# Optimization experiments

Measured on AMD Instinct MI355X. Metric: run time of the kernel, lower is better.

The kernel has to match this reference:

```python
import jax, jax.numpy as jnp
import numpy as np

NEG_NUM = -10000.0


def setup_inputs() -> dict:
    key = jax.random.key(0)
    k1, k2, k3 = jax.random.split(key, 3)
    B, S, T, D = 8, 4096, 512, 1024
    ctx = jax.random.normal(k1, (B, S, D), dtype=jnp.float32)
    query = jax.random.normal(k2, (B, T, D), dtype=jnp.float32)
    mask = jax.random.randint(k3, (B, S), 0, 2, dtype=jnp.int32)
    return {"ctx": ctx, "query": query, "mask": mask}


def reference(ctx, query, mask):
    # ctx: [B, S, D], query: [B, T, D], mask: [B, S] (0 = masked)
    D = query.shape[-1]
    denom = jnp.asarray(np.sqrt(D), dtype=ctx.dtype)
    # scores[b, t, s] = sum_d query[b, t, d] * ctx[b, s, d]
    scores = jnp.einsum("btd,bsd->bts", query, ctx) / denom
    # apply mask per source position (broadcast over target dim)
    scores = jnp.where(mask[:, None, :] == 0, NEG_NUM, scores)
    p_ctx = jax.nn.softmax(scores, axis=-1)  # [B, T, S]
    expected_ctx = jnp.einsum("bts,bsd->btd", p_ctx, ctx)  # [B, T, D]
    return expected_ctx, p_ctx
```

## Files before the change

kernel.cpp:

```cpp
#include <hip/hip_runtime.h>

#define BB 8
#define SS 4096
#define TT 512
#define DD 1024

typedef __attribute__((ext_vector_type(8))) short bf16x8;
typedef __attribute__((ext_vector_type(4))) short bf16x4;
typedef __attribute__((ext_vector_type(4))) float f32x4;

#define GLOAD_LDS16(gp, lp)                                            \
  __builtin_amdgcn_global_load_lds(                                    \
      (const __attribute__((address_space(1))) void*)(gp),             \
      (__attribute__((address_space(3))) void*)(lp), 16, 0, 0)

__device__ inline unsigned short f2bf(float f) {
  unsigned int u = __float_as_uint(f);
  u += 0x7FFFu + ((u >> 16) & 1u);
  return (unsigned short)(u >> 16);
}
__device__ inline void pack16(const float* __restrict__ src, short* __restrict__ dst) {
  f32x4 f0 = *(const f32x4*)(src + 0);
  f32x4 f1 = *(const f32x4*)(src + 4);
  f32x4 f2 = *(const f32x4*)(src + 8);
  f32x4 f3 = *(const f32x4*)(src + 12);
  bf16x8 b0, b1;
  b0[0] = (short)f2bf(f0.x); b0[1] = (short)f2bf(f0.y);
  b0[2] = (short)f2bf(f0.z); b0[3] = (short)f2bf(f0.w);
  b0[4] = (short)f2bf(f1.x); b0[5] = (short)f2bf(f1.y);
  b0[6] = (short)f2bf(f1.z); b0[7] = (short)f2bf(f1.w);
  b1[0] = (short)f2bf(f2.x); b1[1] = (short)f2bf(f2.y);
  b1[2] = (short)f2bf(f2.z); b1[3] = (short)f2bf(f2.w);
  b1[4] = (short)f2bf(f3.x); b1[5] = (short)f2bf(f3.y);
  b1[6] = (short)f2bf(f3.z); b1[7] = (short)f2bf(f3.w);
  *(bf16x8*)(dst + 0) = b0;
  *(bf16x8*)(dst + 8) = b1;
}

#define WS_NEED ((size_t)168 << 20)
#define OFF_QB  ((size_t)0)
#define OFF_CB  ((size_t)8 << 20)
#define OFF_CT  ((size_t)72 << 20)
#define OFF_PB  ((size_t)136 << 20)
#define OFF_PART ((size_t)0)

__global__ __launch_bounds__(256) void prep_q_kernel(const float* __restrict__ q,
                                                     short* __restrict__ qb) {
  const size_t idx = ((size_t)blockIdx.x * 256 + threadIdx.x) * 16;
  pack16(q + idx, qb + idx);
}

__global__ __launch_bounds__(256) void prep_c_kernel(const float* __restrict__ c,
                                                     short* __restrict__ cb,
                                                     short* __restrict__ ct) {
  const int b  = blockIdx.z;
  const int s0 = blockIdx.y * 128;
  const int d0 = blockIdx.x * 64;
  const float* C = c + (size_t)b * SS * DD;
  __shared__ float T[128 * 64];

  const int tid = threadIdx.x;
  const int r0 = tid >> 4;
  const int cc = tid & 15;

  f32x4 v[8];
#pragma unroll
  for (int i = 0; i < 8; ++i)
    v[i] = *(const f32x4*)(C + (size_t)(s0 + r0 + i * 16) * DD + d0 + cc * 4);

#pragma unroll
  for (int i = 0; i < 8; ++i) {
    const int r = r0 + i * 16;
    bf16x4 o;
    o[0] = (short)f2bf(v[i].x); o[1] = (short)f2bf(v[i].y);
    o[2] = (short)f2bf(v[i].z); o[3] = (short)f2bf(v[i].w);
    *(bf16x4*)(cb + (size_t)b * SS * DD + (size_t)(s0 + r) * DD + d0 + cc * 4) = o;
    *(f32x4*)&T[r * 64 + ((cc ^ (r >> 3)) & 15) * 4] = v[i];
  }
  __syncthreads();

  const int sc  = (tid & 15) * 8;
  const int dr0 = tid >> 4;
#pragma unroll
  for (int i = 0; i < 4; ++i) {
    const int d = dr0 + i * 16;
    bf16x8 o;
#pragma unroll
    for (int j = 0; j < 8; ++j) {
      const int s = sc + j;
      o[j] = (short)f2bf(T[s * 64 + (((d >> 2) ^ (s >> 3)) & 15) * 4 + (d & 3)]);
    }
    *(bf16x8*)(ct + (size_t)b * DD * SS + (size_t)(d0 + d) * SS + s0 + sc) = o;
  }
}


__global__ __launch_bounds__(256) void qk_kernel_f(const short* __restrict__ qb,
                                                   const short* __restrict__ cb,
                                                   const int* __restrict__ mask,
                                                   float* __restrict__ p) {
  const int b  = blockIdx.z;
  const int m0 = blockIdx.y * 128;
  const int n0 = blockIdx.x * 128;
  const short* A  = qb + (size_t)b * TT * DD;
  const short* Bt = cb + (size_t)b * SS * DD;

  __shared__ alignas(16) short As[2][128 * 64];
  __shared__ alignas(16) short Bs[2][128 * 64];

  const int tid  = threadIdx.x;
  const int wave = tid >> 6, lane = tid & 63;
  const int quad = lane >> 4, l16 = lane & 15;
  const int wm = (wave >> 1) * 64, wn = (wave & 1) * 64;

  const int rl = lane >> 3;
  const int ck = (lane & 7) ^ (lane >> 3);
  const int x7 = l16 & 7;

  f32x4 acc[4][4];
#pragma unroll
  for (int i = 0; i < 4; ++i)
#pragma unroll
    for (int j = 0; j < 4; ++j) acc[i][j] = (f32x4){0.f, 0.f, 0.f, 0.f};

#define QK_STAGE(buf, k0)                                                     \
  {                                                                           \
    _Pragma("unroll")                                                         \
    for (int t = 0; t < 4; ++t) {                                             \
      const int rb = wave * 32 + t * 8;                                       \
      GLOAD_LDS16(A  + (size_t)(m0 + rb + rl) * DD + (k0) + ck * 8,           \
                  &As[buf][rb * 64]);                                         \
      GLOAD_LDS16(Bt + (size_t)(n0 + rb + rl) * DD + (k0) + ck * 8,           \
                  &Bs[buf][rb * 64]);                                         \
    }                                                                         \
  }

#define QK_COMPUTE(buf)                                                       \
  {                                                                           \
    _Pragma("unroll")                                                         \
    for (int kk = 0; kk < 2; ++kk) {                                          \
      bf16x8 af[4], bfv[4];                                                   \
      _Pragma("unroll")                                                       \
      for (int i = 0; i < 4; ++i)                                             \
        af[i] = *(const bf16x8*)&As[buf][(wm + i * 16 + l16) * 64 +           \
                                        (((kk * 4 + quad) ^ x7) * 8)];        \
      _Pragma("unroll")                                                       \
      for (int j = 0; j < 4; ++j)                                             \
        bfv[j] = *(const bf16x8*)&Bs[buf][(wn + j * 16 + l16) * 64 +          \
                                          (((kk * 4 + quad) ^ x7) * 8)];      \
      _Pragma("unroll")                                                       \
      for (int i = 0; i < 4; ++i)                                             \
        _Pragma("unroll")                                                     \
        for (int j = 0; j < 4; ++j)                                           \
          acc[i][j] = __builtin_amdgcn_mfma_f32_16x16x32_bf16(                \
              af[i], bfv[j], acc[i][j], 0, 0, 0);                             \
    }                                                                         \
  }

  QK_STAGE(0, 0);
  __syncthreads();
  int cur = 0;
  for (int k0 = 64; k0 < DD; k0 += 64) {
    QK_STAGE(cur ^ 1, k0);
    QK_COMPUTE(cur);
    __syncthreads();
    cur ^= 1;
  }
  QK_COMPUTE(cur);

  float* P = p + (size_t)b * TT * SS;
  int mk[4];
#pragma unroll
  for (int j = 0; j < 4; ++j) mk[j] = mask[b * SS + n0 + wn + j * 16 + l16];
#pragma unroll
  for (int i = 0; i < 4; ++i)
#pragma unroll
    for (int j = 0; j < 4; ++j)
#pragma unroll
      for (int r = 0; r < 4; ++r) {
        const int row = m0 + wm + i * 16 + quad * 4 + r;
        const int col = n0 + wn + j * 16 + l16;
        const float val = (mk[j] == 0) ? -10000.0f : acc[i][j][r] * 0.03125f;
        P[(size_t)row * SS + col] = val;
      }
}

__global__ __launch_bounds__(256) void softmax_kernel_f(float* __restrict__ p,
                                                        short* __restrict__ pb) {
  const int wave = threadIdx.x >> 6, lane = threadIdx.x & 63;
  const int row = blockIdx.x * 4 + wave;
  float* pr = p + (size_t)row * SS;
  short* pbr = pb + (size_t)row * SS;

  f32x4 v[16];
  float mx = -3.0e38f;
#pragma unroll
  for (int h = 0; h < 16; ++h) {
    v[h] = *(const f32x4*)(pr + h * 256 + lane * 4);
    mx = fmaxf(mx, fmaxf(fmaxf(v[h].x, v[h].y), fmaxf(v[h].z, v[h].w)));
  }
#pragma unroll
  for (int off = 32; off > 0; off >>= 1) mx = fmaxf(mx, __shfl_xor(mx, off));

  float sum = 0.f;
#pragma unroll
  for (int h = 0; h < 16; ++h) {
    v[h].x = __expf(v[h].x - mx);
    v[h].y = __expf(v[h].y - mx);
    v[h].z = __expf(v[h].z - mx);
    v[h].w = __expf(v[h].w - mx);
    sum += (v[h].x + v[h].y) + (v[h].z + v[h].w);
  }
#pragma unroll
  for (int off = 32; off > 0; off >>= 1) sum += __shfl_xor(sum, off);
  const float inv = 1.0f / sum;

#pragma unroll
  for (int h = 0; h < 16; ++h) {
    f32x4 o;
    o.x = v[h].x * inv; o.y = v[h].y * inv;
    o.z = v[h].z * inv; o.w = v[h].w * inv;
    *(f32x4*)(pr + h * 256 + lane * 4) = o;
    bf16x4 ob;
    ob[0] = (short)f2bf(o.x); ob[1] = (short)f2bf(o.y);
    ob[2] = (short)f2bf(o.z); ob[3] = (short)f2bf(o.w);
    *(bf16x4*)(pbr + h * 256 + lane * 4) = ob;
  }
}

__global__ __launch_bounds__(256) void pv_kernel_f(const short* __restrict__ pb,
                                                   const short* __restrict__ ct,
                                                   float* __restrict__ part) {
  const int n0 = blockIdx.x * 128;
  const int m0 = blockIdx.y * 128;
  const int z  = blockIdx.z;
  const int b  = z >> 1;
  const int ks = z & 1;
  const short* A  = pb + (size_t)b * TT * SS;
  const short* Bt = ct + (size_t)b * DD * SS;

  __shared__ alignas(16) short As[2][128 * 64];
  __shared__ alignas(16) short Bs[2][128 * 64];

  const int tid  = threadIdx.x;
  const int wave = tid >> 6, lane = tid & 63;
  const int quad = lane >> 4, l16 = lane & 15;
  const int wm = (wave >> 1) * 64, wn = (wave & 1) * 64;

  const int rl = lane >> 3;
  const int ck = (lane & 7) ^ (lane >> 3);
  const int x7 = l16 & 7;

  f32x4 acc[4][4];
#pragma unroll
  for (int i = 0; i < 4; ++i)
#pragma unroll
    for (int j = 0; j < 4; ++j) acc[i][j] = (f32x4){0.f, 0.f, 0.f, 0.f};

#define PV_STAGE(buf, k0)                                                     \
  {                                                                           \
    _Pragma("unroll")                                                         \
    for (int t = 0; t < 4; ++t) {                                             \
      const int rb = wave * 32 + t * 8;                                       \
      GLOAD_LDS16(A  + (size_t)(m0 + rb + rl) * SS + (k0) + ck * 8,           \
                  &As[buf][rb * 64]);                                         \
      GLOAD_LDS16(Bt + (size_t)(n0 + rb + rl) * SS + (k0) + ck * 8,           \
                  &Bs[buf][rb * 64]);                                         \
    }                                                                         \
  }

  const int kbeg = ks * 2048;
  const int kend = kbeg + 2048;
  PV_STAGE(0, kbeg);
  __syncthreads();
  int cur = 0;
  for (int k0 = kbeg + 64; k0 < kend; k0 += 64) {
    PV_STAGE(cur ^ 1, k0);
    QK_COMPUTE(cur);
    __syncthreads();
    cur ^= 1;
  }
  QK_COMPUTE(cur);

  float* E = part + (size_t)ks * BB * TT * DD + (size_t)b * TT * DD;
#pragma unroll
  for (int i = 0; i < 4; ++i)
#pragma unroll
    for (int j = 0; j < 4; ++j)
#pragma unroll
      for (int r = 0; r < 4; ++r) {
        const int row = m0 + wm + i * 16 + quad * 4 + r;
        const int col = n0 + wn + j * 16 + l16;
        E[(size_t)row * DD + col] = acc[i][j][r];
      }
}

__global__ __launch_bounds__(256) void reduce_kernel(const float* __restrict__ part,
                                                     float* __restrict__ e) {
  const size_t idx = ((size_t)blockIdx.x * 256 + threadIdx.x) * 4;
  const size_t N = (size_t)BB * TT * DD;
  f32x4 a0 = *(const f32x4*)(part + idx);
  f32x4 a1 = *(const f32x4*)(part + N + idx);
  f32x4 o;
  o.x = a0.x + a1.x;
  o.y = a0.y + a1.y;
  o.z = a0.z + a1.z;
  o.w = a0.w + a1.w;
  *(f32x4*)(e + idx) = o;
}

__global__ __launch_bounds__(256) void qk_kernel(const float* __restrict__ q,
                                                 const float* __restrict__ c,
                                                 float* __restrict__ p) {
  const int b  = blockIdx.z;
  const int m0 = blockIdx.y * 128;
  const int n0 = blockIdx.x * 128;
  const float* A  = q + (size_t)b * TT * DD;
  const float* Bt = c + (size_t)b * SS * DD;
  __shared__ alignas(16) short As[128 * 40];
  __shared__ alignas(16) short Bs[128 * 40];
  const int tid  = threadIdx.x;
  const int wave = tid >> 6, lane = tid & 63;
  const int quad = lane >> 4, l16 = lane & 15;
  const int wm = (wave >> 1) * 64, wn = (wave & 1) * 64;
  f32x4 acc[4][4];
#pragma unroll
  for (int i = 0; i < 4; ++i)
#pragma unroll
    for (int j = 0; j < 4; ++j) acc[i][j] = (f32x4){0.f, 0.f, 0.f, 0.f};
  const int ar = tid >> 1;
  const int ak = (tid & 1) * 16;
  for (int k0 = 0; k0 < DD; k0 += 32) {
    __syncthreads();
    pack16(A  + (size_t)(m0 + ar) * DD + k0 + ak, &As[ar * 40 + ak]);
    pack16(Bt + (size_t)(n0 + ar) * DD + k0 + ak, &Bs[ar * 40 + ak]);
    __syncthreads();
    bf16x8 af[4], bfv[4];
#pragma unroll
  for (int i = 0; i < 4; ++i)
      af[i] = *(const bf16x8*)&As[(wm + i * 16 + l16) * 40 + quad * 8];
#pragma unroll
    for (int j = 0; j < 4; ++j)
      bfv[j] = *(const bf16x8*)&Bs[(wn + j * 16 + l16) * 40 + quad * 8];
#pragma unroll
    for (int i = 0; i < 4; ++i)
#pragma unroll
      for (int j = 0; j < 4; ++j)
        acc[i][j] = __builtin_amdgcn_mfma_f32_16x16x32_bf16(af[i], bfv[j],
                                                            acc[i][j], 0, 0, 0);
  }
  float* P = p + (size_t)b * TT * SS;
#pragma unroll
  for (int i = 0; i < 4; ++i)
#pragma unroll
    for (int j = 0; j < 4; ++j)
#pragma unroll
      for (int r = 0; r < 4; ++r) {
        const int row = m0 + wm + i * 16 + quad * 4 + r;
        const int col = n0 + wn + j * 16 + l16;
        P[(size_t)row * SS + col] = acc[i][j][r] * 0.03125f;
      }
}

__global__ __launch_bounds__(256) void softmax_kernel(float* __restrict__ p,
                                                      const int* __restrict__ mask) {
  const int row = blockIdx.x;
  const int b   = row >> 9;
  float* pr = p + (size_t)row * SS;
  const int* mr = mask + b * SS;
  const int tid = threadIdx.x;
  const int wave = tid >> 6, lane = tid & 63;
  float v[16];
  float mx = -3.0e38f;
#pragma unroll
  for (int h = 0; h < 4; ++h) {
    const int base = tid * 4 + h * 1024;
    f32x4 s = *(const f32x4*)(pr + base);
    const int4 m4 = *(const int4*)(mr + base);
#pragma unroll
    for (int j = 0; j < 4; ++j) {
      float f = (j == 0 ? s.x : j == 1 ? s.y : j == 2 ? s.z : s.w);
      const int mk = (j == 0 ? m4.x : j == 1 ? m4.y : j == 2 ? m4.z : m4.w);
      f = fminf(fmaxf(f, -1.0e30f), 1.0e30f);
      f = (mk == 0) ? -10000.0f : f;
      v[h * 4 + j] = f;
      mx = fmaxf(mx, f);
    }
  }
#pragma unroll
  for (int off = 32; off > 0; off >>= 1) mx = fmaxf(mx, __shfl_down(mx, off));
  __shared__ float red[4];
  if (lane == 0) red[wave] = mx;
  __syncthreads();
  mx = fmaxf(fmaxf(red[0], red[1]), fmaxf(red[2], red[3]));
  __syncthreads();
  float e[16];
  float sum = 0.f;
#pragma unroll
  for (int k = 0; k < 16; ++k) { e[k] = __expf(v[k] - mx); sum += e[k]; }
#pragma unroll
  for (int off = 32; off > 0; off >>= 1) sum += __shfl_down(sum, off);
  if (lane == 0) red[wave] = sum;
  __syncthreads();
  const float inv = 1.0f / (red[0] + red[1] + red[2] + red[3]);
#pragma unroll
  for (int h = 0; h < 4; ++h) {
    const int base = tid * 4 + h * 1024;
    f32x4 o;
    o.x = e[h * 4 + 0] * inv; o.y = e[h * 4 + 1] * inv;
    o.z = e[h * 4 + 2] * inv; o.w = e[h * 4 + 3] * inv;
    *(f32x4*)(pr + base) = o;
  }
}

__global__ __launch_bounds__(256) void pv_kernel(const float* __restrict__ p,
                                                 const float* __restrict__ c,
                                                 float* __restrict__ e) {
  const int b  = blockIdx.z;
  const int m0 = blockIdx.y * 128;
  const int n0 = blockIdx.x * 128;
  const float* A  = p + (size_t)b * TT * SS;
  const float* Bm = c + (size_t)b * SS * DD;
  __shared__ alignas(16) short As[128 * 40];
  __shared__ alignas(16) short Bs[128 * 40];
  const int tid  = threadIdx.x;
  const int wave = tid >> 6, lane = tid & 63;
  const int quad = lane >> 4, l16 = lane & 15;
  const int wm = (wave >> 1) * 64, wn = (wave & 1) * 64;
  f32x4 acc[4][4];
#pragma unroll
  for (int i = 0; i < 4; ++i)
#pragma unroll
    for (int j = 0; j < 4; ++j) acc[i][j] = (f32x4){0.f, 0.f, 0.f, 0.f};
  const int ar = tid >> 1;
  const int ak = (tid & 1) * 16;
  const int kk = tid >> 3;
  const int c0 = (tid & 7) * 16;
  for (int k0 = 0; k0 < SS; k0 += 32) {
    __syncthreads();
    pack16(A + (size_t)(m0 + ar) * SS + k0 + ak, &As[ar * 40 + ak]);
    {
      const float* bp = Bm + (size_t)(k0 + kk) * DD + n0 + c0;
#pragma unroll
      for (int h = 0; h < 4; ++h) {
        f32x4 f = *(const f32x4*)(bp + h * 4);
        Bs[(c0 + h * 4 + 0) * 40 + kk] = (short)f2bf(f.x);
        Bs[(c0 + h * 4 + 1) * 40 + kk] = (short)f2bf(f.y);
        Bs[(c0 + h * 4 + 2) * 40 + kk] = (short)f2bf(f.z);
        Bs[(c0 + h * 4 + 3) * 40 + kk] = (short)f2bf(f.w);
      }
    }
    __syncthreads();
    bf16x8 af[4], bfv[4];
#pragma unroll
    for (int i = 0; i < 4; ++i)
      af[i] = *(const bf16x8*)&As[(wm + i * 16 + l16) * 40 + quad * 8];
#pragma unroll
    for (int j = 0; j < 4; ++j)
      bfv[j] = *(const bf16x8*)&Bs[(wn + j * 16 + l16) * 40 + quad * 8];
#pragma unroll
    for (int i = 0; i < 4; ++i)
#pragma unroll
      for (int j = 0; j < 4; ++j)
        acc[i][j] = __builtin_amdgcn_mfma_f32_16x16x32_bf16(af[i], bfv[j],
                                                            acc[i][j], 0, 0, 0);
  }
  float* E = e + (size_t)b * TT * DD;
#pragma unroll
  for (int i = 0; i < 4; ++i)
#pragma unroll
    for (int j = 0; j < 4; ++j)
#pragma unroll
      for (int r = 0; r < 4; ++r) {
        const int row = m0 + wm + i * 16 + quad * 4 + r;
        const int col = n0 + wn + j * 16 + l16;
        E[(size_t)row * DD + col] = acc[i][j][r];
      }
}

extern "C" void kernel_launch(void* const* d_in, const int* in_sizes, int n_in,
                              void* d_out, int out_size, void* d_ws, size_t ws_size,
                              hipStream_t stream) {
  const float* ctx   = (const float*)d_in[0];
  const float* query = (const float*)d_in[1];
  const int*   mask  = (const int*)d_in[2];

  float* expected = (float*)d_out;
  float* p        = (float*)d_out + (size_t)BB * TT * DD;

  if (ws_size >= WS_NEED) {
    char* ws = (char*)d_ws;
    short* qb = (short*)(ws + OFF_QB);
    short* cb = (short*)(ws + OFF_CB);
    short* ct = (short*)(ws + OFF_CT);
    short* pb = (short*)(ws + OFF_PB);
    float* part = (float*)(ws + OFF_PART);

    prep_q_kernel<<<dim3((BB * TT * DD) / (256 * 16)), 256, 0, stream>>>(query, qb);
    prep_c_kernel<<<dim3(DD / 64, SS / 128, BB), 256, 0, stream>>>(ctx, cb, ct);
    qk_kernel_f<<<dim3(SS / 128, TT / 128, BB), 256, 0, stream>>>(qb, cb, mask, p);
    softmax_kernel_f<<<dim3((BB * TT) / 4), 256, 0, stream>>>(p, pb);
    pv_kernel_f<<<dim3(DD / 128, TT / 128, BB * 2), 256, 0, stream>>>(pb, ct, part);
    reduce_kernel<<<dim3((BB * TT * DD) / (256 * 4)), 256, 0, stream>>>(part, expected);
  } else {
    qk_kernel<<<dim3(SS / 128, TT / 128, BB), 256, 0, stream>>>(query, ctx, p);
    softmax_kernel<<<dim3(BB * TT), 256, 0, stream>>>(p, mask);
    pv_kernel<<<dim3(DD / 128, TT / 128, BB), 256, 0, stream>>>(p, ctx, expected);
  }
}
```

Baseline: 399.3 us.

## Drop transposed ctx copy; read row-major V via LDS transpose loads in PV

Removes the transposed bf16 copy of ctx that the prep step built and simplifies prep to a plain fp32-to-bf16 pack. The PV GEMM now stages row-major V tiles into LDS and uses ds_read_b64_tr_b16 transposing reads to form the MFMA B operand. This cuts a 64MB transposed write and its LDS transpose work, but relies on correct tr-load addressing and adds an explicit lgkmcnt wait plus a sched barrier inside the compute loop.

```diff
diff --git a/kernel.cpp b/kernel.cpp
--- a/kernel.cpp
+++ b/kernel.cpp
@@ -40,9 +40,8 @@
 #define WS_NEED ((size_t)168 << 20)
 #define OFF_QB  ((size_t)0)
 #define OFF_CB  ((size_t)8 << 20)
-#define OFF_CT  ((size_t)72 << 20)
+#define OFF_PART ((size_t)72 << 20)
 #define OFF_PB  ((size_t)136 << 20)
-#define OFF_PART ((size_t)0)
 
 __global__ __launch_bounds__(256) void prep_q_kernel(const float* __restrict__ q,
                                                      short* __restrict__ qb) {
@@ -50,48 +49,10 @@
   pack16(q + idx, qb + idx);
 }
 
-__global__ __launch_bounds__(256) void prep_c_kernel(const float* __restrict__ c,
-                                                     short* __restrict__ cb,
-                                                     short* __restrict__ ct) {
-  const int b  = blockIdx.z;
-  const int s0 = blockIdx.y * 128;
-  const int d0 = blockIdx.x * 64;
-  const float* C = c + (size_t)b * SS * DD;
-  __shared__ float T[128 * 64];
-
-  const int tid = threadIdx.x;
-  const int r0 = tid >> 4;
-  const int cc = tid & 15;
-
-  f32x4 v[8];
-#pragma unroll
-  for (int i = 0; i < 8; ++i)
-    v[i] = *(const f32x4*)(C + (size_t)(s0 + r0 + i * 16) * DD + d0 + cc * 4);
-
-#pragma unroll
-  for (int i = 0; i < 8; ++i) {
-    const int r = r0 + i * 16;
-    bf16x4 o;
-    o[0] = (short)f2bf(v[i].x); o[1] = (short)f2bf(v[i].y);
-    o[2] = (short)f2bf(v[i].z); o[3] = (short)f2bf(v[i].w);
-    *(bf16x4*)(cb + (size_t)b * SS * DD + (size_t)(s0 + r) * DD + d0 + cc * 4) = o;
-    *(f32x4*)&T[r * 64 + ((cc ^ (r >> 3)) & 15) * 4] = v[i];
-  }
-  __syncthreads();
-
-  const int sc  = (tid & 15) * 8;
-  const int dr0 = tid >> 4;
-#pragma unroll
-  for (int i = 0; i < 4; ++i) {
-    const int d = dr0 + i * 16;
-    bf16x8 o;
-#pragma unroll
-    for (int j = 0; j < 8; ++j) {
-      const int s = sc + j;
-      o[j] = (short)f2bf(T[s * 64 + (((d >> 2) ^ (s >> 3)) & 15) * 4 + (d & 3)]);
-    }
-    *(bf16x8*)(ct + (size_t)b * DD * SS + (size_t)(d0 + d) * SS + s0 + sc) = o;
-  }
+__global__ __launch_bounds__(256) void prep_cb_kernel(const float* __restrict__ c,
+                                                      short* __restrict__ cb) {
+  const size_t idx = ((size_t)blockIdx.x * 256 + threadIdx.x) * 16;
+  pack16(c + idx, cb + idx);
 }
 
 
@@ -229,18 +190,18 @@
 }
 
 __global__ __launch_bounds__(256) void pv_kernel_f(const short* __restrict__ pb,
-                                                   const short* __restrict__ ct,
+                                                   const short* __restrict__ cb,
                                                    float* __restrict__ part) {
   const int n0 = blockIdx.x * 128;
   const int m0 = blockIdx.y * 128;
   const int z  = blockIdx.z;
   const int b  = z >> 1;
   const int ks = z & 1;
-  const short* A  = pb + (size_t)b * TT * SS;
-  const short* Bt = ct + (size_t)b * DD * SS;
+  const short* A   = pb + (size_t)b * TT * SS;
+  const short* Vrm = cb + (size_t)b * SS * DD;
 
   __shared__ alignas(16) short As[2][128 * 64];
-  __shared__ alignas(16) short Bs[2][128 * 64];
+  __shared__ alignas(16) short Bs[2][64 * 128];
 
   const int tid  = threadIdx.x;
   const int wave = tid >> 6, lane = tid & 63;
@@ -250,6 +211,12 @@
   const int rl = lane >> 3;
   const int ck = (lane & 7) ^ (lane >> 3);
   const int x7 = l16 & 7;
+
+  const int rB  = (lane & 7) >> 1;
+  const int dB  = (lane >> 3) * 16 + (lane & 1) * 8;
+
+  const unsigned ldsB0 = (unsigned)(unsigned long long)&Bs[0][0];
+  const unsigned baseBq = ldsB0 + (unsigned)(quad * 2048 + (wave & 1) * 512 + l16 * 8);
 
   f32x4 acc[4][4];
 #pragma unroll
@@ -262,10 +229,41 @@
     _Pragma("unroll")                                                         \
     for (int t = 0; t < 4; ++t) {                                             \
       const int rb = wave * 32 + t * 8;                                       \
-      GLOAD_LDS16(A  + (size_t)(m0 + rb + rl) * SS + (k0) + ck * 8,           \
+      GLOAD_LDS16(A + (size_t)(m0 + rb + rl) * SS + (k0) + ck * 8,            \
                   &As[buf][rb * 64]);                                         \
-      GLOAD_LDS16(Bt + (size_t)(n0 + rb + rl) * SS + (k0) + ck * 8,           \
-                  &Bs[buf][rb * 64]);                                         \
+      const int kg = wave * 4 + t;                        \
+      GLOAD_LDS16(Vrm + (size_t)((k0) + kg * 4 + rB) * DD + n0 + dB,          \
+                  &Bs[buf][kg * 512]);                                        \
+    }                                                                         \
+  }
+
+#define PV_COMPUTE(buf)                                                       \
+  {                                                                           \
+    const unsigned bb = baseBq + (unsigned)(buf) * 16384u;                    \
+    _Pragma("unroll")                                                         \
+    for (int kk = 0; kk < 2; ++kk) {                                          \
+      bf16x8 af[4];                                                           \
+      _Pragma("unroll")                                                       \
+      for (int i = 0; i < 4; ++i)                                             \
+        af[i] = *(const bf16x8*)&As[buf][(wm + i * 16 + l16) * 64 +           \
+                                        (((kk * 4 + quad) ^ x7) * 8)];        \
+      union { struct { int2 lo, hi; } p; bf16x8 v; } bu[4];                   \
+      _Pragma("unroll")                                                       \
+      for (int j = 0; j < 4; ++j) {                                           \
+        const unsigned aj = bb + (unsigned)(kk * 8192 + j * 128);             \
+        asm volatile("ds_read_b64_tr_b16 %0, %1"                              \
+                     : "=v"(bu[j].p.lo) : "v"(aj) : "memory");                \
+        asm volatile("ds_read_b64_tr_b16 %0, %1 offset:1024"                  \
+                     : "=v"(bu[j].p.hi) : "v"(aj) : "memory");                \
+      }                                                                       \
+      asm volatile("s_waitcnt lgkmcnt(0)" ::: "memory");                      \
+      __builtin_amdgcn_sched_barrier(0);                                      \
+      _Pragma("unroll")                                                       \
+      for (int i = 0; i < 4; ++i)                                             \
+        _Pragma("unroll")                                                     \
+        for (int j = 0; j < 4; ++j)                                           \
+          acc[i][j] = __builtin_amdgcn_mfma_f32_16x16x32_bf16(                \
+              af[i], bu[j].v, acc[i][j], 0, 0, 0);                            \
     }                                                                         \
   }
 
@@ -276,11 +274,11 @@
   int cur = 0;
   for (int k0 = kbeg + 64; k0 < kend; k0 += 64) {
     PV_STAGE(cur ^ 1, k0);
-    QK_COMPUTE(cur);
+    PV_COMPUTE(cur);
     __syncthreads();
     cur ^= 1;
   }
-  QK_COMPUTE(cur);
+  PV_COMPUTE(cur);
 
   float* E = part + (size_t)ks * BB * TT * DD + (size_t)b * TT * DD;
 #pragma unroll
@@ -492,15 +490,14 @@
     char* ws = (char*)d_ws;
     short* qb = (short*)(ws + OFF_QB);
     short* cb = (short*)(ws + OFF_CB);
-    short* ct = (short*)(ws + OFF_CT);
     short* pb = (short*)(ws + OFF_PB);
     float* part = (float*)(ws + OFF_PART);
 
     prep_q_kernel<<<dim3((BB * TT * DD) / (256 * 16)), 256, 0, stream>>>(query, qb);
-    prep_c_kernel<<<dim3(DD / 64, SS / 128, BB), 256, 0, stream>>>(ctx, cb, ct);
+    prep_cb_kernel<<<dim3((BB * SS * DD) / (256 * 16)), 256, 0, stream>>>(ctx, cb);
     qk_kernel_f<<<dim3(SS / 128, TT / 128, BB), 256, 0, stream>>>(qb, cb, mask, p);
     softmax_kernel_f<<<dim3((BB * TT) / 4), 256, 0, stream>>>(p, pb);
-    pv_kernel_f<<<dim3(DD / 128, TT / 128, BB * 2), 256, 0, stream>>>(pb, ct, part);
+    pv_kernel_f<<<dim3(DD / 128, TT / 128, BB * 2), 256, 0, stream>>>(pb, cb, part);
     reduce_kernel<<<dim3((BB * TT * DD) / (256 * 4)), 256, 0, stream>>>(part, expected);
   } else {
     qk_kernel<<<dim3(SS / 128, TT / 128, BB), 256, 0, stream>>>(query, ctx, p);
```

Measured after the change: 357.1 us. -10.6%, faster.
